# Kernel tuning notes

Measured on AMD Instinct MI355X. Metric: run time of the kernel, lower is better.

Reference implementation:

```python
import jax, jax.numpy as jnp
import numpy as np

B, T, K = 64, 1024, 128
START, STOP = K - 2, K - 1  # tag_dictionary['<START>'], tag_dictionary['<STOP>']
NEG = -10000.0


def setup_inputs() -> dict:
    key = jax.random.key(0)
    k1, k2, k3, k4 = jax.random.split(key, 4)
    feats = jax.random.normal(k1, (B, T, K), jnp.float32)
    tags = jax.random.randint(k2, (B, T), 0, K - 2)          # real labels only
    lens = jax.random.randint(k3, (B,), 1, T + 1)            # 1 <= len <= T
    transitions = jax.random.normal(k4, (K, K), jnp.float32)
    transitions = transitions.at[START, :].set(NEG).at[:, STOP].set(NEG)
    return {"feats": feats, "tags": tags, "lens": lens, "transitions": transitions}


def _forward_alg(feats, transitions, lens):
    # feats: [B, T, K]; CRF forward (log-partition) via scan over time.
    B_, T_, K_ = feats.shape
    # init: only START position kept from feats[:, 0, :], rest -10000
    alpha0 = jnp.full((B_, K_), NEG, feats.dtype).at[:, START].set(feats[:, 0, START])

    def step(alpha, feat_i):
        # tag_var[b, s, p] = feat_i[b, s] + transitions[s, p] + alpha[b, p]
        new = feat_i + jax.scipy.special.logsumexp(alpha[:, None, :] + transitions[None, :, :], axis=2)
        return new, new

    _, alphas = jax.lax.scan(step, alpha0, jnp.swapaxes(feats[:, 1:, :], 0, 1))  # [T-1, B, K]
    all_alphas = jnp.concatenate([alpha0[None], alphas], axis=0)  # [T, B, K]; idx t-1 == forward_var[:, t]
    terminal = all_alphas[lens - 1, jnp.arange(B_)]               # [B, K]
    return jax.scipy.special.logsumexp(terminal, axis=1)          # [B]


def _score_sentence(feats, transitions, tags, lens):
    B_, T_, K_ = feats.shape
    pos = jnp.arange(T_ - 1)
    # pad_stop_tags = tags[:, 1:] with positions >= len-1 replaced by STOP
    stop_tags = jnp.where(pos[None, :] >= (lens - 1)[:, None], STOP, tags[:, 1:])
    trans_sc = transitions[stop_tags, tags[:, :-1]]               # [B, T-1]
    tmask = (pos[None, :] < (lens - 1)[:, None]).astype(feats.dtype)
    emit = jnp.take_along_axis(feats, tags[:, :, None], axis=2)[:, :, 0]  # [B, T]
    emask = (jnp.arange(T_)[None, :] < lens[:, None]).astype(feats.dtype)
    return jnp.sum(trans_sc * tmask, axis=1) + jnp.sum(emit * emask, axis=1)


def reference(feats, tags, lens, transitions):
    forward_score = _forward_alg(feats, transitions, lens)
    gold_score = _score_sentence(feats, transitions, tags, lens)
    return jnp.mean(forward_score - gold_score)
```

## Files before the change

kernel.cpp:

```cpp
#include <hip/hip_runtime.h>
#include <math.h>

#define BB 64
#define TT 1024
#define KK 128
#define START_TAG 126
#define STOP_TAG 127
#define NTHREADS 512
#define CS 64

typedef float v2f __attribute__((ext_vector_type(2)));

__global__ __launch_bounds__(NTHREADS) void crf_forward(
    const float* __restrict__ feats,
    const int*   __restrict__ tags,
    const int*   __restrict__ lens,
    const float* __restrict__ trans,
    float*       __restrict__ out_pb)
{
  __shared__ float Tld[KK][KK + 1];
  __shared__ __align__(16) float e_lds[KK];
  __shared__ float partial[NTHREADS];
  __shared__ float maxT_lds[KK];
  __shared__ __align__(16) float Fbuf[CS * KK];
  __shared__ float wsum[NTHREADS / 64];

  const int tid = threadIdx.x;
  const int b   = blockIdx.x;
  const int j   = tid & (KK - 1);
  const int q   = tid >> 7;
  const int L   = lens[b];
  const float* fb = feats + (size_t)b * TT * KK;

  for (int i = tid; i < KK * KK; i += NTHREADS)
    Tld[i >> 7][i & (KK - 1)] = trans[i];
  __syncthreads();

  float mT = -INFINITY;
  #pragma unroll
  for (int i = 0; i < 32; ++i) mT = fmaxf(mT, Tld[j][q * 32 + i]);
  partial[tid] = mT;
  __syncthreads();
  const float maxTj = fmaxf(fmaxf(partial[j], partial[j + 128]),
                            fmaxf(partial[j + 256], partial[j + 384]));
  v2f Er2[16];
  #pragma unroll
  for (int i = 0; i < 16; ++i) {
    Er2[i][0] = __expf(Tld[j][q * 32 + 2 * i]     - maxTj);
    Er2[i][1] = __expf(Tld[j][q * 32 + 2 * i + 1] - maxTj);
  }
  __syncthreads();
  if (q == 0) maxT_lds[j] = maxTj;

  if (tid < KK) e_lds[tid] = (tid == START_TAG) ? 1.0f : 0.0f;
  float M = fb[START_TAG];
  __syncthreads();

  const int j0 = (tid * 16) & (KK - 1);
  float4 mTv[4];
  #pragma unroll
  for (int i = 0; i < 4; ++i) mTv[i] = ((const float4*)maxT_lds)[(j0 >> 2) + i];

  float4 pf[4];
  {
    const float4* src = (const float4*)fb;
    #pragma unroll
    for (int i = 0; i < 4; ++i) pf[i] = src[tid * 4 + i];
  }

  for (int c = 0; c * CS < L; ++c) {
    float4* Fb4 = (float4*)Fbuf;
    #pragma unroll
    for (int i = 0; i < 4; ++i) {
      float4 v = pf[i];
      float4 m = mTv[i];
      float4 o;
      o.x = __expf(v.x + m.x); o.y = __expf(v.y + m.y);
      o.z = __expf(v.z + m.z); o.w = __expf(v.w + m.w);
      Fb4[tid * 4 + i] = o;
    }
    if ((c + 1) * CS < TT) {
      const float4* src = (const float4*)(fb + (size_t)(c + 1) * CS * KK);
      #pragma unroll
      for (int i = 0; i < 4; ++i) pf[i] = src[tid * 4 + i];
    }
    __syncthreads();

    const int t_begin = (c == 0) ? 1 : c * CS;
    const int t_end   = (L < (c + 1) * CS) ? L : (c + 1) * CS;
    for (int t = t_begin; t < t_end; ++t) {
      const v2f* e2 = (const v2f*)(e_lds + q * 32);
      v2f a0 = {0.f, 0.f}, a1 = {0.f, 0.f}, a2 = {0.f, 0.f}, a3 = {0.f, 0.f};
      #pragma unroll
      for (int i = 0; i < 4; ++i) {
        a0 += e2[4 * i + 0] * Er2[4 * i + 0];
        a1 += e2[4 * i + 1] * Er2[4 * i + 1];
        a2 += e2[4 * i + 2] * Er2[4 * i + 2];
        a3 += e2[4 * i + 3] * Er2[4 * i + 3];
      }
      v2f asum = (a0 + a1) + (a2 + a3);
      float F = Fbuf[(t & (CS - 1)) * KK + j];
      partial[tid] = asum[0] + asum[1];
      __syncthreads();

      if (q == 0) {
        float d = (partial[j]       + partial[j + 128]) +
                  (partial[j + 256] + partial[j + 384]);
        float s = (partial[START_TAG]       + partial[START_TAG + 128]) +
                  (partial[START_TAG + 256] + partial[START_TAG + 384]);
        float r;
        asm("v_rcp_f32 %0, %1" : "=v"(r) : "v"(s));
        e_lds[j] = d * F * r;
        if (tid < 64) M += __logf(s);
      }
      __syncthreads();
    }
  }

  float fwd = 0.f;
  if (tid < 64) {
    float sm = e_lds[tid] + e_lds[tid + 64];
    #pragma unroll
    for (int m = 1; m < 64; m <<= 1) sm += __shfl_xor(sm, m, 64);
    fwd = M + __logf(sm);
  }

  float g = 0.f;
  const int* tg = tags + b * TT;
  for (int t = tid; t < TT; t += NTHREADS) {
    if (t < L)     g += fb[(size_t)t * KK + tg[t]];
    if (t < L - 1) g += Tld[tg[t + 1]][tg[t]];
  }
  #pragma unroll
  for (int m = 1; m < 64; m <<= 1) g += __shfl_xor(g, m, 64);
  if ((tid & 63) == 0) wsum[tid >> 6] = g;
  __syncthreads();
  if (tid == 0) {
    float gold = 0.f;
    #pragma unroll
    for (int w = 0; w < NTHREADS / 64; ++w) gold += wsum[w];
    out_pb[b] = fwd - gold;
  }
}

__global__ void crf_mean(const float* __restrict__ pb, float* __restrict__ out) {
  int tid = threadIdx.x;
  float v = pb[tid];
  #pragma unroll
  for (int m = 1; m < 64; m <<= 1) v += __shfl_xor(v, m, 64);
  if (tid == 0) out[0] = v * (1.0f / 64.0f);
}

extern "C" void kernel_launch(void* const* d_in, const int* in_sizes, int n_in,
                              void* d_out, int out_size, void* d_ws, size_t ws_size,
                              hipStream_t stream) {
  const float* feats = (const float*)d_in[0];
  const int*   tags  = (const int*)d_in[1];
  const int*   lens  = (const int*)d_in[2];
  const float* trans = (const float*)d_in[3];
  float* pb = (float*)d_ws;
  crf_forward<<<BB, NTHREADS, 0, stream>>>(feats, tags, lens, trans, pb);
  crf_mean<<<1, 64, 0, stream>>>(pb, (float*)d_out);
}
```

Baseline: 448.8 us.

## Use DPP quad reductions and double-buffered alpha to halve per-step barriers

The block shrinks to 256 threads, and each group of 4 lanes now owns two target tags. The partial sums over source tags are combined with DPP quad shuffles instead of a shared-memory partial array, so each time step needs one barrier instead of two. The alpha vector is double-buffered in padded LDS rows, and the normalizer is read from the previous step's buffer. Each thread now holds twice as many exp-transition registers and does twice the FMA work per step, which may raise register pressure.

```diff
diff --git a/kernel.cpp b/kernel.cpp
--- a/kernel.cpp
+++ b/kernel.cpp
@@ -6,10 +6,24 @@
 #define KK 128
 #define START_TAG 126
 #define STOP_TAG 127
-#define NTHREADS 512
+#define NTHREADS 256
 #define CS 64
+#define EP 36
 
 typedef float v2f __attribute__((ext_vector_type(2)));
+
+__device__ __forceinline__ float quad_add(float x) {
+  int y = __builtin_amdgcn_update_dpp(0, __float_as_int(x), 0xB1, 0xF, 0xF, true);
+  x = x + __int_as_float(y);
+  y = __builtin_amdgcn_update_dpp(0, __float_as_int(x), 0x4E, 0xF, 0xF, true);
+  return x + __int_as_float(y);
+}
+__device__ __forceinline__ float quad_max(float x) {
+  int y = __builtin_amdgcn_update_dpp(0, __float_as_int(x), 0xB1, 0xF, 0xF, true);
+  x = fmaxf(x, __int_as_float(y));
+  y = __builtin_amdgcn_update_dpp(0, __float_as_int(x), 0x4E, 0xF, 0xF, true);
+  return fmaxf(x, __int_as_float(y));
+}
 
 __global__ __launch_bounds__(NTHREADS) void crf_forward(
     const float* __restrict__ feats,
@@ -19,127 +33,150 @@
     float*       __restrict__ out_pb)
 {
   __shared__ float Tld[KK][KK + 1];
-  __shared__ __align__(16) float e_lds[KK];
-  __shared__ float partial[NTHREADS];
+  __shared__ __align__(16) float ebuf[2][4 * EP];
+  __shared__ float sbuf[2];
   __shared__ float maxT_lds[KK];
   __shared__ __align__(16) float Fbuf[CS * KK];
   __shared__ float wsum[NTHREADS / 64];
 
   const int tid = threadIdx.x;
   const int b   = blockIdx.x;
-  const int j   = tid & (KK - 1);
-  const int q   = tid >> 7;
+  const int q   = tid & 3;
+  const int g   = tid >> 2;
+  const int r0  = 2 * g;
   const int L   = lens[b];
   const float* fb = feats + (size_t)b * TT * KK;
 
-  for (int i = tid; i < KK * KK; i += NTHREADS)
-    Tld[i >> 7][i & (KK - 1)] = trans[i];
+  for (int i = tid; i < KK * KK / 4; i += NTHREADS) {
+    float4 v = ((const float4*)trans)[i];
+    int rr = i >> 5, cc = (i & 31) * 4;
+    Tld[rr][cc] = v.x; Tld[rr][cc + 1] = v.y; Tld[rr][cc + 2] = v.z; Tld[rr][cc + 3] = v.w;
+  }
   __syncthreads();
 
-  float mT = -INFINITY;
-  #pragma unroll
-  for (int i = 0; i < 32; ++i) mT = fmaxf(mT, Tld[j][q * 32 + i]);
-  partial[tid] = mT;
-  __syncthreads();
-  const float maxTj = fmaxf(fmaxf(partial[j], partial[j + 128]),
-                            fmaxf(partial[j + 256], partial[j + 384]));
-  v2f Er2[16];
+  float m0 = -INFINITY, m1 = -INFINITY;
+  #pragma unroll
+  for (int i = 0; i < 32; ++i) {
+    m0 = fmaxf(m0, Tld[r0][q * 32 + i]);
+    m1 = fmaxf(m1, Tld[r0 + 1][q * 32 + i]);
+  }
+  m0 = quad_max(m0);
+  m1 = quad_max(m1);
+  v2f Ea[16], Eb[16];
   #pragma unroll
   for (int i = 0; i < 16; ++i) {
-    Er2[i][0] = __expf(Tld[j][q * 32 + 2 * i]     - maxTj);
-    Er2[i][1] = __expf(Tld[j][q * 32 + 2 * i + 1] - maxTj);
-  }
-  __syncthreads();
-  if (q == 0) maxT_lds[j] = maxTj;
-
-  if (tid < KK) e_lds[tid] = (tid == START_TAG) ? 1.0f : 0.0f;
+    Ea[i][0] = __expf(Tld[r0][q * 32 + 2 * i]         - m0);
+    Ea[i][1] = __expf(Tld[r0][q * 32 + 2 * i + 1]     - m0);
+    Eb[i][0] = __expf(Tld[r0 + 1][q * 32 + 2 * i]     - m1);
+    Eb[i][1] = __expf(Tld[r0 + 1][q * 32 + 2 * i + 1] - m1);
+  }
+  if (q == 0) { maxT_lds[r0] = m0; maxT_lds[r0 + 1] = m1; }
+
+  if (tid < KK)
+    ebuf[0][(tid >> 5) * EP + (tid & 31)] = (tid == START_TAG) ? 1.0f : 0.0f;
+  if (tid == 0) sbuf[0] = 1.0f;
   float M = fb[START_TAG];
   __syncthreads();
 
-  const int j0 = (tid * 16) & (KK - 1);
-  float4 mTv[4];
-  #pragma unroll
-  for (int i = 0; i < 4; ++i) mTv[i] = ((const float4*)maxT_lds)[(j0 >> 2) + i];
-
-  float4 pf[4];
+  const int j0 = (tid * 32) & (KK - 1);
+  float4 mTv[8];
+  #pragma unroll
+  for (int i = 0; i < 8; ++i) mTv[i] = ((const float4*)maxT_lds)[(j0 >> 2) + i];
+
+  float4 pf[8];
   {
     const float4* src = (const float4*)fb;
     #pragma unroll
-    for (int i = 0; i < 4; ++i) pf[i] = src[tid * 4 + i];
-  }
-
+    for (int i = 0; i < 8; ++i) pf[i] = src[tid * 8 + i];
+  }
+
+  int p = 0;
   for (int c = 0; c * CS < L; ++c) {
     float4* Fb4 = (float4*)Fbuf;
     #pragma unroll
-    for (int i = 0; i < 4; ++i) {
-      float4 v = pf[i];
-      float4 m = mTv[i];
+    for (int i = 0; i < 8; ++i) {
+      float4 v = pf[i], mm = mTv[i];
       float4 o;
-      o.x = __expf(v.x + m.x); o.y = __expf(v.y + m.y);
-      o.z = __expf(v.z + m.z); o.w = __expf(v.w + m.w);
-      Fb4[tid * 4 + i] = o;
+      o.x = __expf(v.x + mm.x); o.y = __expf(v.y + mm.y);
+      o.z = __expf(v.z + mm.z); o.w = __expf(v.w + mm.w);
+      Fb4[tid * 8 + i] = o;
     }
     if ((c + 1) * CS < TT) {
       const float4* src = (const float4*)(fb + (size_t)(c + 1) * CS * KK);
       #pragma unroll
-      for (int i = 0; i < 4; ++i) pf[i] = src[tid * 4 + i];
+      for (int i = 0; i < 8; ++i) pf[i] = src[tid * 8 + i];
     }
     __syncthreads();
 
     const int t_begin = (c == 0) ? 1 : c * CS;
     const int t_end   = (L < (c + 1) * CS) ? L : (c + 1) * CS;
     for (int t = t_begin; t < t_end; ++t) {
-      const v2f* e2 = (const v2f*)(e_lds + q * 32);
-      v2f a0 = {0.f, 0.f}, a1 = {0.f, 0.f}, a2 = {0.f, 0.f}, a3 = {0.f, 0.f};
+      const float* er = ebuf[p];
+      float* ew = ebuf[p ^ 1];
+      const float sp = sbuf[p];
+      const v2f Fv = *(const v2f*)(Fbuf + (t & (CS - 1)) * KK + r0);
+      float rr;
+      asm("v_rcp_f32 %0, %1" : "=v"(rr) : "v"(sp));
+      const float rF0 = rr * Fv[0];
+      const float rF1 = rr * Fv[1];
+
+      const v2f* ep2 = (const v2f*)(er + q * EP);
+      v2f a0 = {0.f,0.f}, a1 = {0.f,0.f}, a2 = {0.f,0.f}, a3 = {0.f,0.f};
+      v2f b0 = {0.f,0.f}, b1 = {0.f,0.f}, b2 = {0.f,0.f}, b3 = {0.f,0.f};
       #pragma unroll
       for (int i = 0; i < 4; ++i) {
-        a0 += e2[4 * i + 0] * Er2[4 * i + 0];
-        a1 += e2[4 * i + 1] * Er2[4 * i + 1];
-        a2 += e2[4 * i + 2] * Er2[4 * i + 2];
-        a3 += e2[4 * i + 3] * Er2[4 * i + 3];
+        v2f e0 = ep2[4 * i + 0], e1 = ep2[4 * i + 1];
+        v2f e2 = ep2[4 * i + 2], e3 = ep2[4 * i + 3];
+        a0 += e0 * Ea[4 * i + 0];
+        a1 += e1 * Ea[4 * i + 1];
+        a2 += e2 * Ea[4 * i + 2];
+        a3 += e3 * Ea[4 * i + 3];
+        b0 += e0 * Eb[4 * i + 0];
+        b1 += e1 * Eb[4 * i + 1];
+        b2 += e2 * Eb[4 * i + 2];
+        b3 += e3 * Eb[4 * i + 3];
       }
-      v2f asum = (a0 + a1) + (a2 + a3);
-      float F = Fbuf[(t & (CS - 1)) * KK + j];
-      partial[tid] = asum[0] + asum[1];
+      v2f as = (a0 + a1) + (a2 + a3);
+      v2f bs = (b0 + b1) + (b2 + b3);
+      float d0 = quad_add(as[0] + as[1]);
+      float d1 = quad_add(bs[0] + bs[1]);
+
+      v2f ev; ev[0] = d0 * rF0; ev[1] = d1 * rF1;
+      *(v2f*)(ew + (r0 >> 5) * EP + (r0 & 31)) = ev;
+      if (g == 63) sbuf[p ^ 1] = d0;
+      if (tid < 64) M += __logf(sp);
+      p ^= 1;
       __syncthreads();
-
-      if (q == 0) {
-        float d = (partial[j]       + partial[j + 128]) +
-                  (partial[j + 256] + partial[j + 384]);
-        float s = (partial[START_TAG]       + partial[START_TAG + 128]) +
-                  (partial[START_TAG + 256] + partial[START_TAG + 384]);
-        float r;
-        asm("v_rcp_f32 %0, %1" : "=v"(r) : "v"(s));
-        e_lds[j] = d * F * r;
-        if (tid < 64) M += __logf(s);
-      }
-      __syncthreads();
     }
   }
 
   float fwd = 0.f;
-  if (tid < 64) {
-    float sm = e_lds[tid] + e_lds[tid + 64];
-    #pragma unroll
-    for (int m = 1; m < 64; m <<= 1) sm += __shfl_xor(sm, m, 64);
-    fwd = M + __logf(sm);
-  }
-
-  float g = 0.f;
+  {
+    const float* efin = ebuf[p];
+    if (tid < 64) {
+      float sm = efin[(tid >> 5) * EP + (tid & 31)]
+               + efin[((tid + 64) >> 5) * EP + ((tid + 64) & 31)];
+      #pragma unroll
+      for (int m = 1; m < 64; m <<= 1) sm += __shfl_xor(sm, m, 64);
+      fwd = M + __logf(sm);
+    }
+  }
+
+  float gold = 0.f;
   const int* tg = tags + b * TT;
   for (int t = tid; t < TT; t += NTHREADS) {
-    if (t < L)     g += fb[(size_t)t * KK + tg[t]];
-    if (t < L - 1) g += Tld[tg[t + 1]][tg[t]];
-  }
-  #pragma unroll
-  for (int m = 1; m < 64; m <<= 1) g += __shfl_xor(g, m, 64);
-  if ((tid & 63) == 0) wsum[tid >> 6] = g;
+    if (t < L)     gold += fb[(size_t)t * KK + tg[t]];
+    if (t < L - 1) gold += Tld[tg[t + 1]][tg[t]];
+  }
+  #pragma unroll
+  for (int m = 1; m < 64; m <<= 1) gold += __shfl_xor(gold, m, 64);
+  if ((tid & 63) == 0) wsum[tid >> 6] = gold;
   __syncthreads();
   if (tid == 0) {
-    float gold = 0.f;
+    float gs = 0.f;
     #pragma unroll
-    for (int w = 0; w < NTHREADS / 64; ++w) gold += wsum[w];
-    out_pb[b] = fwd - gold;
+    for (int w = 0; w < NTHREADS / 64; ++w) gs += wsum[w];
+    out_pb[b] = fwd - gs;
   }
 }
 
```

Measured after the change: 429.6 us, median of 2. -4.3%, faster.

## Run CRF forward recursion in a single wavefront with register-resident exp(transitions)

Applied to the files above, without the earlier changes.

Each batch now uses one 64-lane wavefront instead of 512 threads. Each lane owns two target tags and holds their full exp(transition) rows in registers (256 floats). The cross-thread partial-sum LDS reduction and the two __syncthreads per timestep go away. Each step instead reads the shared alpha vector from LDS, broadcasts the normaliser via readlane, and prefetches emissions four steps ahead directly from global memory. The trade-off is very high register pressure and 8x less parallelism per timestep, with possible spills and longer dot products per lane.

```diff
diff --git a/kernel.cpp b/kernel.cpp
--- a/kernel.cpp
+++ b/kernel.cpp
@@ -6,141 +6,108 @@
 #define KK 128
 #define START_TAG 126
 #define STOP_TAG 127
-#define NTHREADS 512
-#define CS 64
 
 typedef float v2f __attribute__((ext_vector_type(2)));
+typedef float v4f __attribute__((ext_vector_type(4)));
 
-__global__ __launch_bounds__(NTHREADS) void crf_forward(
+__global__ __launch_bounds__(64, 1) void crf_forward(
     const float* __restrict__ feats,
     const int*   __restrict__ tags,
     const int*   __restrict__ lens,
     const float* __restrict__ trans,
     float*       __restrict__ out_pb)
 {
-  __shared__ float Tld[KK][KK + 1];
   __shared__ __align__(16) float e_lds[KK];
-  __shared__ float partial[NTHREADS];
-  __shared__ float maxT_lds[KK];
-  __shared__ __align__(16) float Fbuf[CS * KK];
-  __shared__ float wsum[NTHREADS / 64];
 
-  const int tid = threadIdx.x;
-  const int b   = blockIdx.x;
-  const int j   = tid & (KK - 1);
-  const int q   = tid >> 7;
-  const int L   = lens[b];
+  const int l  = threadIdx.x;
+  const int b  = blockIdx.x;
+  const int r0 = 2 * l;
+  const int L  = lens[b];
   const float* fb = feats + (size_t)b * TT * KK;
 
-  for (int i = tid; i < KK * KK; i += NTHREADS)
-    Tld[i >> 7][i & (KK - 1)] = trans[i];
-  __syncthreads();
-
-  float mT = -INFINITY;
-  #pragma unroll
-  for (int i = 0; i < 32; ++i) mT = fmaxf(mT, Tld[j][q * 32 + i]);
-  partial[tid] = mT;
-  __syncthreads();
-  const float maxTj = fmaxf(fmaxf(partial[j], partial[j + 128]),
-                            fmaxf(partial[j + 256], partial[j + 384]));
-  v2f Er2[16];
-  #pragma unroll
-  for (int i = 0; i < 16; ++i) {
-    Er2[i][0] = __expf(Tld[j][q * 32 + 2 * i]     - maxTj);
-    Er2[i][1] = __expf(Tld[j][q * 32 + 2 * i + 1] - maxTj);
+  float mT0 = -INFINITY, mT1 = -INFINITY;
+  {
+    const v4f* t0 = (const v4f*)(trans + (size_t)r0 * KK);
+    const v4f* t1 = (const v4f*)(trans + (size_t)(r0 + 1) * KK);
+    #pragma unroll
+    for (int i = 0; i < 32; ++i) {
+      v4f a = t0[i], c = t1[i];
+      mT0 = fmaxf(mT0, fmaxf(fmaxf(a[0], a[1]), fmaxf(a[2], a[3])));
+      mT1 = fmaxf(mT1, fmaxf(fmaxf(c[0], c[1]), fmaxf(c[2], c[3])));
+    }
   }
-  __syncthreads();
-  if (q == 0) maxT_lds[j] = maxTj;
-
-  if (tid < KK) e_lds[tid] = (tid == START_TAG) ? 1.0f : 0.0f;
-  float M = fb[START_TAG];
-  __syncthreads();
-
-  const int j0 = (tid * 16) & (KK - 1);
-  float4 mTv[4];
-  #pragma unroll
-  for (int i = 0; i < 4; ++i) mTv[i] = ((const float4*)maxT_lds)[(j0 >> 2) + i];
-
-  float4 pf[4];
+  v4f E0[32], E1[32];
   {
-    const float4* src = (const float4*)fb;
+    const v4f* t0 = (const v4f*)(trans + (size_t)r0 * KK);
+    const v4f* t1 = (const v4f*)(trans + (size_t)(r0 + 1) * KK);
     #pragma unroll
-    for (int i = 0; i < 4; ++i) pf[i] = src[tid * 4 + i];
-  }
-
-  for (int c = 0; c * CS < L; ++c) {
-    float4* Fb4 = (float4*)Fbuf;
-    #pragma unroll
-    for (int i = 0; i < 4; ++i) {
-      float4 v = pf[i];
-      float4 m = mTv[i];
-      float4 o;
-      o.x = __expf(v.x + m.x); o.y = __expf(v.y + m.y);
-      o.z = __expf(v.z + m.z); o.w = __expf(v.w + m.w);
-      Fb4[tid * 4 + i] = o;
-    }
-    if ((c + 1) * CS < TT) {
-      const float4* src = (const float4*)(fb + (size_t)(c + 1) * CS * KK);
-      #pragma unroll
-      for (int i = 0; i < 4; ++i) pf[i] = src[tid * 4 + i];
-    }
-    __syncthreads();
-
-    const int t_begin = (c == 0) ? 1 : c * CS;
-    const int t_end   = (L < (c + 1) * CS) ? L : (c + 1) * CS;
-    for (int t = t_begin; t < t_end; ++t) {
-      const v2f* e2 = (const v2f*)(e_lds + q * 32);
-      v2f a0 = {0.f, 0.f}, a1 = {0.f, 0.f}, a2 = {0.f, 0.f}, a3 = {0.f, 0.f};
-      #pragma unroll
-      for (int i = 0; i < 4; ++i) {
-        a0 += e2[4 * i + 0] * Er2[4 * i + 0];
-        a1 += e2[4 * i + 1] * Er2[4 * i + 1];
-        a2 += e2[4 * i + 2] * Er2[4 * i + 2];
-        a3 += e2[4 * i + 3] * Er2[4 * i + 3];
-      }
-      v2f asum = (a0 + a1) + (a2 + a3);
-      float F = Fbuf[(t & (CS - 1)) * KK + j];
-      partial[tid] = asum[0] + asum[1];
-      __syncthreads();
-
-      if (q == 0) {
-        float d = (partial[j]       + partial[j + 128]) +
-                  (partial[j + 256] + partial[j + 384]);
-        float s = (partial[START_TAG]       + partial[START_TAG + 128]) +
-                  (partial[START_TAG + 256] + partial[START_TAG + 384]);
-        float r;
-        asm("v_rcp_f32 %0, %1" : "=v"(r) : "v"(s));
-        e_lds[j] = d * F * r;
-        if (tid < 64) M += __logf(s);
-      }
-      __syncthreads();
+    for (int i = 0; i < 32; ++i) {
+      v4f a = t0[i], c = t1[i], o, p;
+      o[0] = __expf(a[0] - mT0); o[1] = __expf(a[1] - mT0);
+      o[2] = __expf(a[2] - mT0); o[3] = __expf(a[3] - mT0);
+      p[0] = __expf(c[0] - mT1); p[1] = __expf(c[1] - mT1);
+      p[2] = __expf(c[2] - mT1); p[3] = __expf(c[3] - mT1);
+      E0[i] = o; E1[i] = p;
     }
   }
 
-  float fwd = 0.f;
-  if (tid < 64) {
-    float sm = e_lds[tid] + e_lds[tid + 64];
+  v2f ev; ev[0] = (l == 63) ? 1.0f : 0.0f; ev[1] = 0.0f;
+  *(v2f*)(e_lds + r0) = ev;
+  float M = fb[START_TAG];
+  float s_prev = 1.0f, r = 1.0f;
+
+  v2f p0 = *(const v2f*)(fb + (size_t)1 * KK + r0);
+  v2f p1 = *(const v2f*)(fb + (size_t)2 * KK + r0);
+  v2f p2 = *(const v2f*)(fb + (size_t)3 * KK + r0);
+  v2f p3 = *(const v2f*)(fb + (size_t)4 * KK + r0);
+
+  #pragma unroll 4
+  for (int t = 1; t < L; ++t) {
+    float rF0 = __expf(p0[0] + mT0) * r;
+    float rF1 = __expf(p0[1] + mT1) * r;
+    p0 = p1; p1 = p2; p2 = p3;
+    {
+      int tn = t + 4; tn = (tn < TT) ? tn : (TT - 1);
+      p3 = *(const v2f*)(fb + (size_t)tn * KK + r0);
+    }
+
+    const v4f* eb = (const v4f*)e_lds;
+    v4f a0 = {0.f,0.f,0.f,0.f}, a1 = a0, a2 = a0, a3 = a0;
+    v4f c0 = a0, c1 = a0, c2 = a0, c3 = a0;
     #pragma unroll
-    for (int m = 1; m < 64; m <<= 1) sm += __shfl_xor(sm, m, 64);
-    fwd = M + __logf(sm);
+    for (int i = 0; i < 8; ++i) {
+      v4f e0 = eb[4*i], e1 = eb[4*i+1], e2 = eb[4*i+2], e3 = eb[4*i+3];
+      a0 += e0 * E0[4*i];   a1 += e1 * E0[4*i+1];
+      a2 += e2 * E0[4*i+2]; a3 += e3 * E0[4*i+3];
+      c0 += e0 * E1[4*i];   c1 += e1 * E1[4*i+1];
+      c2 += e2 * E1[4*i+2]; c3 += e3 * E1[4*i+3];
+    }
+    v4f av = (a0 + a1) + (a2 + a3);
+    v4f cv = (c0 + c1) + (c2 + c3);
+    float d0 = (av[0] + av[1]) + (av[2] + av[3]);
+    float d1 = (cv[0] + cv[1]) + (cv[2] + cv[3]);
+
+    M += __logf(s_prev);
+    ev[0] = d0 * rF0; ev[1] = d1 * rF1;
+    s_prev = __int_as_float(__builtin_amdgcn_readlane(__float_as_int(d0), 63));
+    r = __builtin_amdgcn_rcpf(s_prev);
+    *(v2f*)(e_lds + r0) = ev;
   }
+
+  float sm = ev[0] + ev[1];
+  #pragma unroll
+  for (int m = 1; m < 64; m <<= 1) sm += __shfl_xor(sm, m, 64);
+  const float fwd = M + __logf(sm);
 
   float g = 0.f;
   const int* tg = tags + b * TT;
-  for (int t = tid; t < TT; t += NTHREADS) {
+  for (int t = l; t < TT; t += 64) {
     if (t < L)     g += fb[(size_t)t * KK + tg[t]];
-    if (t < L - 1) g += Tld[tg[t + 1]][tg[t]];
+    if (t < L - 1) g += trans[(size_t)tg[t + 1] * KK + tg[t]];
   }
   #pragma unroll
   for (int m = 1; m < 64; m <<= 1) g += __shfl_xor(g, m, 64);
-  if ((tid & 63) == 0) wsum[tid >> 6] = g;
-  __syncthreads();
-  if (tid == 0) {
-    float gold = 0.f;
-    #pragma unroll
-    for (int w = 0; w < NTHREADS / 64; ++w) gold += wsum[w];
-    out_pb[b] = fwd - gold;
-  }
+  if (l == 0) out_pb[b] = fwd - g;
 }
 
 __global__ void crf_mean(const float* __restrict__ pb, float* __restrict__ out) {
@@ -159,6 +126,6 @@
   const int*   lens  = (const int*)d_in[2];
   const float* trans = (const float*)d_in[3];
   float* pb = (float*)d_ws;
-  crf_forward<<<BB, NTHREADS, 0, stream>>>(feats, tags, lens, trans, pb);
+  crf_forward<<<BB, 64, 0, stream>>>(feats, tags, lens, trans, pb);
   crf_mean<<<1, 64, 0, stream>>>(pb, (float*)d_out);
 }
```

New measurement: 1.500 ms. 3.34x slower.
